# Kernel tuning notes

Measured on AMD Instinct MI355X. Metric: run time of the kernel, lower is better.

Reference implementation:

```python
import jax, jax.numpy as jnp
import numpy as np

N_GAUSS = 3200          # 20*20*8 voxel-center pseudo points
FEAT_DIM = 17
RENDER_H, RENDER_W = 48, 88
GT_H, GT_W = 192, 352
VOXEL_SIZE = 0.8
PC_MIN = np.array([-8.0, -8.0, -3.2], np.float32)
PC_MAX = np.array([8.0, 8.0, 3.2], np.float32)
NUSC_FREQ = np.array([1163161, 2309034, 188743, 2997643, 20317180, 852476, 243808,
                      2457947, 497017, 2731022, 7224789, 214411435, 5565043,
                      63191967, 76098082, 128860031, 141625221, 2307405309], np.float64)


def setup_inputs() -> dict:
    key = jax.random.key(0)
    k1, k2 = jax.random.split(key, 2)
    # pseudo voxel-center grid (get_presudo_xyz): cell centers on a 20x20x8 grid
    gx = (np.arange(20) + 0.5) * VOXEL_SIZE + PC_MIN[0]
    gy = (np.arange(20) + 0.5) * VOXEL_SIZE + PC_MIN[1]
    gz = (np.arange(8) + 0.5) * VOXEL_SIZE + PC_MIN[2]
    X, Y, Z = np.meshgrid(gx, gy, gz, indexing='ij')
    pc_xyz = np.stack([X, Y, Z], -1).reshape(-1, 3).astype(np.float32)
    # distCUDA2 on a regular grid: mean sq dist to 3 NNs == voxel_size^2
    scales = np.full((N_GAUSS, 3), np.log(VOXEL_SIZE), np.float32)  # log(sqrt(v^2))
    rots = np.zeros((N_GAUSS, 4), np.float32); rots[:, 0] = 1.0  # identity quats
    # two cameras looking at the grid (z_cam > 0 for all points)
    vm0 = np.array([[1, 0, 0, 0], [0, -1, 0, 0], [0, 0, -1, 20], [0, 0, 0, 1]], np.float32)
    vm1 = np.array([[0, 1, 0, 0], [0, 0, -1, 0], [-1, 0, 0, 20], [0, 0, 0, 1]], np.float32)
    viewmats = np.stack([vm0, vm1])
    intr = np.array([[100.0, 50.0, RENDER_W / 2.0, RENDER_H / 2.0]] * 2, np.float32)
    cw = (1.0 / np.log(NUSC_FREQ[:17] + 0.001)).astype(np.float32)
    return {
        'voxel_feats': jax.random.normal(k1, (1, N_GAUSS, FEAT_DIM), jnp.float32),
        'opacity': jax.random.uniform(k2, (1, N_GAUSS, 1), jnp.float32),
        'pc_xyz': jnp.asarray(pc_xyz),
        'scales': jnp.asarray(scales),
        'rots': jnp.asarray(rots),
        'viewmats': jnp.asarray(viewmats),
        'intrinsics': jnp.asarray(intr),
        'class_weights': jnp.asarray(cw),
        'gt_sem': jax.random.randint(jax.random.fold_in(key, 1), (2, GT_H, GT_W), 0, 17, jnp.int32),
        'sem_mask': jax.random.randint(jax.random.fold_in(key, 2), (2, GT_H, GT_W), 0, 2, jnp.int32),
    }


def quat_to_rot(q):
    q = q / jnp.linalg.norm(q, axis=-1, keepdims=True)
    w, x, y, z = q[:, 0], q[:, 1], q[:, 2], q[:, 3]
    return jnp.stack([
        jnp.stack([1 - 2 * (y * y + z * z), 2 * (x * y - w * z), 2 * (x * z + w * y)], -1),
        jnp.stack([2 * (x * y + w * z), 1 - 2 * (x * x + z * z), 2 * (y * z - w * x)], -1),
        jnp.stack([2 * (x * z - w * y), 2 * (y * z + w * x), 1 - 2 * (x * x + y * y)], -1),
    ], -2)  # [N,3,3]


def nearest_resize(img, H, W):
    hi, wi = img.shape
    ri = (jnp.arange(H) * hi) // H
    ci = (jnp.arange(W) * wi) // W
    return img[ri][:, ci]


def render_feature_map(feats, opac, xyz, scale, Rq, viewmat, intr):
    fx, fy, cx, cy = intr[0], intr[1], intr[2], intr[3]
    Rw, t = viewmat[:3, :3], viewmat[:3, 3]
    p = xyz @ Rw.T + t                      # [N,3] camera-frame
    z = p[:, 2]
    valid = z > 0.2
    zc = jnp.maximum(z, 0.2)
    u = fx * p[:, 0] / zc + cx
    v = fy * p[:, 1] / zc + cy
    # 3D covariance: Rq diag(s^2) Rq^T, then to camera frame
    cov3d = jnp.einsum('nij,nj,nkj->nik', Rq, scale * scale, Rq)
    cov_c = jnp.einsum('ij,njk,lk->nil', Rw, cov3d, Rw)
    # projection Jacobian (EWA splatting)
    zero = jnp.zeros_like(zc)
    J = jnp.stack([
        jnp.stack([fx / zc, zero, -fx * p[:, 0] / (zc * zc)], -1),
        jnp.stack([zero, fy / zc, -fy * p[:, 1] / (zc * zc)], -1),
    ], -2)                                  # [N,2,3]
    cov2 = jnp.einsum('nij,njk,nlk->nil', J, cov_c, J)
    a = cov2[:, 0, 0] + 0.3
    b = cov2[:, 0, 1]
    c = cov2[:, 1, 1] + 0.3
    det = jnp.maximum(a * c - b * b, 1e-8)
    A, B, C = c / det, -b / det, a / det    # conic
    px = jnp.arange(RENDER_W, dtype=jnp.float32)
    py = jnp.arange(RENDER_H, dtype=jnp.float32)
    dx = px[None, :] - u[:, None]           # [N,W]
    dy = py[None, :] - v[:, None]           # [N,H]
    power = (-0.5 * (A[:, None, None] * dx[:, None, :] ** 2
                     + C[:, None, None] * dy[:, :, None] ** 2)
             - B[:, None, None] * dx[:, None, :] * dy[:, :, None])  # [N,H,W]
    power = jnp.minimum(power, 0.0)
    alpha = jnp.clip(opac[:, None, None] * jnp.exp(power), 0.0, 0.99)
    alpha = alpha * valid[:, None, None].astype(alpha.dtype)
    order = jnp.argsort(z)                  # front-to-back depth sort
    alpha = alpha[order]
    feats_s = feats[order]
    T = jnp.cumprod(1.0 - alpha, axis=0)
    T_excl = jnp.concatenate([jnp.ones_like(T[:1]), T[:-1]], axis=0)
    w = alpha * T_excl                      # composite weights [N,H,W]
    return jnp.einsum('nhw,nc->hwc', w, feats_s)  # [H,W,17]


def masked_weighted_ce(logits, gt, mask, cw):
    logp = jax.nn.log_softmax(logits, -1)
    nll = -jnp.take_along_axis(logp, gt[:, None], axis=1)[:, 0]
    wi = cw[gt] * mask
    return jnp.sum(wi * nll) / jnp.maximum(jnp.sum(wi), 1e-8)


def reference(voxel_feats, opacity, pc_xyz, scales, rots, viewmats, intrinsics,
              class_weights, gt_sem, sem_mask):
    scale = jnp.exp(scales)
    Rq = quat_to_rot(rots)
    B = voxel_feats.shape[0]
    n_cam = viewmats.shape[0]
    loss_batch = 0.0
    for b in range(B):
        feats = voxel_feats[b].reshape(-1, FEAT_DIM)
        opac = opacity[b].reshape(-1)
        loss_cam = 0.0
        for c in range(n_cam):
            img = render_feature_map(feats, opac, pc_xyz, scale, Rq,
                                     viewmats[c], intrinsics[c])
            logits = img.reshape(-1, FEAT_DIM)
            gt = nearest_resize(gt_sem[c], RENDER_H, RENDER_W).reshape(-1)
            m = nearest_resize(sem_mask[c], RENDER_H, RENDER_W).reshape(-1).astype(jnp.float32)
            loss_cam = loss_cam + masked_weighted_ce(logits, gt, m, class_weights)
        loss_batch = loss_batch + loss_cam / n_cam
    return loss_batch / B  # gaussian_sem_weight = 1.0
```

## Files before the change

### kernel.cpp

```cpp
#include <hip/hip_runtime.h>

#define NG 3200
#define NF 17
#define NFP 18
#define RH 48
#define RW 88
#define NPIX (RH*RW)
#define GTH 192
#define GTW 352
#define NCAM 2
#define CHUNK 64
#define NCHUNK 50
#define GPC 5
#define NGROUP 10
#define NPL 9

typedef float v2f __attribute__((ext_vector_type(2)));
typedef _Float16 h2 __attribute__((ext_vector_type(2)));

#define Z_OFF    0
#define PU_OFF   (Z_OFF + NCAM*NG)
#define PS_OFF   (PU_OFF + NCAM*NG*6)
#define FS_OFF   (PS_OFF + NCAM*NG*6)
#define PT_OFF   (FS_OFF + NCAM*NG*NFP)
#define GP_OFF   (PT_OFF + NCAM*NCHUNK*NPL*NPIX)
#define ACC_OFF  (GP_OFF + NCAM*NGROUP*NPL*NPIX)

__global__ __launch_bounds__(256) void k_preproc(
    const float* __restrict__ opac, const float* __restrict__ xyz,
    const float* __restrict__ scales, const float* __restrict__ rots,
    const float* __restrict__ vm, const float* __restrict__ intr,
    float* __restrict__ ws)
{
  int idx = blockIdx.x*blockDim.x + threadIdx.x;
  if (idx < 4) ws[ACC_OFF + idx] = 0.0f;
  if (idx >= NCAM*NG) return;
  int cam = idx / NG, g = idx % NG;

  float qw=rots[g*4+0], qx=rots[g*4+1], qy=rots[g*4+2], qz=rots[g*4+3];
  float qn = rsqrtf(qw*qw+qx*qx+qy*qy+qz*qz);
  qw*=qn; qx*=qn; qy*=qn; qz*=qn;
  float R[3][3];
  R[0][0]=1.f-2.f*(qy*qy+qz*qz); R[0][1]=2.f*(qx*qy-qw*qz); R[0][2]=2.f*(qx*qz+qw*qy);
  R[1][0]=2.f*(qx*qy+qw*qz); R[1][1]=1.f-2.f*(qx*qx+qz*qz); R[1][2]=2.f*(qy*qz-qw*qx);
  R[2][0]=2.f*(qx*qz-qw*qy); R[2][1]=2.f*(qy*qz+qw*qx); R[2][2]=1.f-2.f*(qx*qx+qy*qy);

  float s2[3];
  #pragma unroll
  for (int k=0;k<3;k++){ float s=expf(scales[g*3+k]); s2[k]=s*s; }

  float M[3][3];
  #pragma unroll
  for(int i=0;i<3;i++)
    #pragma unroll
    for(int j=0;j<3;j++)
      M[i][j] = R[i][0]*s2[0]*R[j][0] + R[i][1]*s2[1]*R[j][1] + R[i][2]*s2[2]*R[j][2];

  const float* Vm = vm + cam*16;
  float Rw[3][3], t[3];
  #pragma unroll
  for(int i=0;i<3;i++){
    #pragma unroll
    for(int j=0;j<3;j++) Rw[i][j]=Vm[i*4+j];
    t[i]=Vm[i*4+3];
  }

  float T1[3][3];
  #pragma unroll
  for(int i=0;i<3;i++)
    #pragma unroll
    for(int j=0;j<3;j++)
      T1[i][j] = Rw[i][0]*M[0][j] + Rw[i][1]*M[1][j] + Rw[i][2]*M[2][j];
  float V[3][3];
  #pragma unroll
  for(int i=0;i<3;i++)
    #pragma unroll
    for(int j=0;j<3;j++)
      V[i][j] = T1[i][0]*Rw[j][0] + T1[i][1]*Rw[j][1] + T1[i][2]*Rw[j][2];

  float X=xyz[g*3+0], Y=xyz[g*3+1], Zp=xyz[g*3+2];
  float p0 = Rw[0][0]*X + Rw[0][1]*Y + Rw[0][2]*Zp + t[0];
  float p1 = Rw[1][0]*X + Rw[1][1]*Y + Rw[1][2]*Zp + t[1];
  float p2 = Rw[2][0]*X + Rw[2][1]*Y + Rw[2][2]*Zp + t[2];

  float z  = p2;
  float zc = fmaxf(z, 0.2f);
  float fx=intr[cam*4+0], fy=intr[cam*4+1], cx=intr[cam*4+2], cy=intr[cam*4+3];
  float u = fx*p0/zc + cx;
  float v = fy*p1/zc + cy;

  float j00 = fx/zc, j02 = -fx*p0/(zc*zc);
  float j11 = fy/zc, j12 = -fy*p1/(zc*zc);
  float c00 = j00*j00*V[0][0] + 2.f*j00*j02*V[0][2] + j02*j02*V[2][2];
  float c01 = j00*(V[0][1]*j11 + V[0][2]*j12) + j02*(V[2][1]*j11 + V[2][2]*j12);
  float c11 = j11*j11*V[1][1] + 2.f*j11*j12*V[1][2] + j12*j12*V[2][2];

  float a = c00 + 0.3f, b = c01, c = c11 + 0.3f;
  float det = fmaxf(a*c - b*b, 1e-8f);
  const float L2E = 1.4426950408889634f;
  float A2 = -0.5f*L2E * (c/det);
  float B2 = -L2E * (-b/det);
  float C2 = -0.5f*L2E * (a/det);
  float opv = (z > 0.2f) ? opac[g] : 0.0f;

  ws[Z_OFF + idx] = z;
  float* P = ws + PU_OFF + (size_t)idx*6;
  P[0]=u; P[1]=v; P[2]=A2; P[3]=B2; P[4]=C2; P[5]=opv;
}

__global__ __launch_bounds__(256) void k_sort(
    const float* __restrict__ feats, float* __restrict__ ws)
{
  __shared__ float zsh[NG];
  int cam = blockIdx.y;
  for (int i=threadIdx.x; i<NG; i+=256) zsh[i] = ws[Z_OFF + cam*NG + i];
  __syncthreads();

  int wave = threadIdx.x >> 6, lane = threadIdx.x & 63;
  int g = blockIdx.x*4 + wave;
  float zi = zsh[g];
  int rank = 0;
  #pragma unroll 5
  for (int k=0; k<NG/64; k++){
    int j = k*64 + lane;
    float zj = zsh[j];
    rank += ((zj < zi) || (zj == zi && j < g)) ? 1 : 0;
  }
  #pragma unroll
  for (int off=32; off>0; off>>=1) rank += __shfl_down(rank, off, 64);
  rank = __shfl(rank, 0, 64);

  const float* src = ws + PU_OFF + (size_t)(cam*NG+g)*6;
  if (lane < 6) (ws + PS_OFF + (size_t)(cam*NG+rank)*6)[lane] = src[lane];
  if (lane < NFP) (ws + FS_OFF + (size_t)(cam*NG+rank)*NFP)[lane] =
                     (lane < NF) ? feats[g*NF+lane] : 0.0f;
}

__global__ __launch_bounds__(192) void k_render(float* __restrict__ ws)
{
  __shared__ float sp[CHUNK*6];
  __shared__ v2f   sf2[CHUNK*(NFP/2)];
  int cam = blockIdx.z, chunk = blockIdx.y;
  int g0 = chunk*CHUNK;
  const float* psrc = ws + PS_OFF + (size_t)(cam*NG+g0)*6;
  for (int i=threadIdx.x; i<CHUNK*6; i+=192) sp[i]=psrc[i];
  const float* fsrc = ws + FS_OFF + (size_t)(cam*NG+g0)*NFP;
  float* sff = (float*)sf2;
  for (int i=threadIdx.x; i<CHUNK*NFP; i+=192) sff[i]=fsrc[i];
  __syncthreads();

  int pix = blockIdx.x*192 + threadIdx.x;
  float px = (float)(pix % RW), py = (float)(pix / RW);

  float T = 1.0f;
  v2f F2[9];
  #pragma unroll
  for(int k=0;k<9;k++) F2[k]=(v2f)(0.f);

  #pragma unroll 4
  for (int g=0; g<CHUNK; g++){
    const float* P = sp + g*6;
    float dx = px - P[0], dy = py - P[1];
    float m1 = P[2]*dx;
    float m2 = fmaf(P[3], dy, m1);
    float m3 = dx*m2;
    float power2 = fmaf(P[4]*dy, dy, m3);
    power2 = fminf(power2, 0.f);
    float alpha = fminf(P[5]*exp2f(power2), 0.99f);
    float w = alpha*T;
    T = fmaf(-alpha, T, T);
    v2f w2; w2.x = w; w2.y = w;
    const v2f* f2 = sf2 + g*(NFP/2);
    #pragma unroll
    for(int k=0;k<9;k++) F2[k] += w2*f2[k];
  }

  const float* Ff = (const float*)F2;
  h2* out = (h2*)(ws + PT_OFF) + (size_t)((cam*NCHUNK+chunk)*NPL)*NPIX + pix;
  #pragma unroll
  for(int k=0;k<8;k++){
    h2 v; v.x = (_Float16)Ff[2*k]; v.y = (_Float16)Ff[2*k+1];
    out[k*NPIX] = v;
  }
  { h2 v; v.x = (_Float16)Ff[16]; v.y = (_Float16)T; out[8*NPIX] = v; }
}

__global__ __launch_bounds__(192) void k_combine(float* __restrict__ ws)
{
  int cam = blockIdx.z, grp = blockIdx.y;
  int pix = blockIdx.x*192 + threadIdx.x;
  float F[NF];
  #pragma unroll
  for(int k=0;k<NF;k++) F[k]=0.f;
  float T = 1.f;
  for (int c=grp*GPC; c<grp*GPC+GPC; c++){
    const h2* base = (const h2*)(ws + PT_OFF) + (size_t)((cam*NCHUNK+c)*NPL)*NPIX + pix;
    h2 v[9];
    #pragma unroll
    for(int k=0;k<9;k++) v[k] = base[k*NPIX];
    #pragma unroll
    for(int k=0;k<8;k++){ F[2*k] += T*(float)v[k].x; F[2*k+1] += T*(float)v[k].y; }
    F[16] += T*(float)v[8].x;
    T *= (float)v[8].y;
  }
  h2* out = (h2*)(ws + GP_OFF) + (size_t)((cam*NGROUP+grp)*NPL)*NPIX + pix;
  #pragma unroll
  for(int k=0;k<8;k++){
    h2 v; v.x = (_Float16)F[2*k]; v.y = (_Float16)F[2*k+1];
    out[k*NPIX] = v;
  }
  { h2 v; v.x = (_Float16)F[16]; v.y = (_Float16)T; out[8*NPIX] = v; }
}

__global__ __launch_bounds__(192) void k_loss(
    const int* __restrict__ gt, const int* __restrict__ mask,
    const float* __restrict__ cw, float* __restrict__ ws)
{
  int cam = blockIdx.y;
  int pix = blockIdx.x*192 + threadIdx.x;
  float img[NF];
  #pragma unroll
  for(int k=0;k<NF;k++) img[k]=0.f;
  float Trun = 1.f;
  for (int c=0; c<NGROUP; c++){
    const h2* base = (const h2*)(ws + GP_OFF) + (size_t)((cam*NGROUP+c)*NPL)*NPIX + pix;
    h2 v[9];
    #pragma unroll
    for(int k=0;k<9;k++) v[k] = base[k*NPIX];
    #pragma unroll
    for(int k=0;k<8;k++){ img[2*k] += Trun*(float)v[k].x; img[2*k+1] += Trun*(float)v[k].y; }
    img[16] += Trun*(float)v[8].x;
    Trun *= (float)v[8].y;
  }
  int row = pix / RW, col = pix % RW;
  int gofs = cam*GTH*GTW + (row*4)*GTW + col*4;
  int gi = gt[gofs];
  float mi = (float)mask[gofs];
  float mx = img[0];
  #pragma unroll
  for(int k=1;k<NF;k++) mx = fmaxf(mx, img[k]);
  float s = 0.f;
  #pragma unroll
  for(int k=0;k<NF;k++) s += expf(img[k]-mx);
  float lse = mx + logf(s);
  float nll = lse - img[gi];
  float wi  = cw[gi]*mi;
  float num = wi*nll, den = wi;
  #pragma unroll
  for (int off=32; off>0; off>>=1){
    num += __shfl_down(num, off, 64);
    den += __shfl_down(den, off, 64);
  }
  if ((threadIdx.x & 63) == 0){
    atomicAdd(ws + ACC_OFF + cam*2 + 0, num);
    atomicAdd(ws + ACC_OFF + cam*2 + 1, den);
  }
}

__global__ void k_final(const float* __restrict__ ws, float* __restrict__ out)
{
  float l0 = ws[ACC_OFF+0]/fmaxf(ws[ACC_OFF+1], 1e-8f);
  float l1 = ws[ACC_OFF+2]/fmaxf(ws[ACC_OFF+3], 1e-8f);
  out[0] = 0.5f*(l0 + l1);
}

extern "C" void kernel_launch(void* const* d_in, const int* in_sizes, int n_in,
                              void* d_out, int out_size, void* d_ws, size_t ws_size,
                              hipStream_t stream) {
  const float* vf   = (const float*)d_in[0];
  const float* op   = (const float*)d_in[1];
  const float* xyz  = (const float*)d_in[2];
  const float* sc   = (const float*)d_in[3];
  const float* rt   = (const float*)d_in[4];
  const float* vm   = (const float*)d_in[5];
  const float* intr = (const float*)d_in[6];
  const float* cw   = (const float*)d_in[7];
  const int*   gt   = (const int*)d_in[8];
  const int*   mask = (const int*)d_in[9];
  float* ws  = (float*)d_ws;
  float* out = (float*)d_out;

  k_preproc<<<dim3((NCAM*NG+255)/256), 256, 0, stream>>>(op, xyz, sc, rt, vm, intr, ws);
  k_sort   <<<dim3(NG/4, NCAM), 256, 0, stream>>>(vf, ws);
  k_render <<<dim3(NPIX/192, NCHUNK, NCAM), 192, 0, stream>>>(ws);
  k_combine<<<dim3(NPIX/192, NGROUP, NCAM), 192, 0, stream>>>(ws);
  k_loss   <<<dim3(NPIX/192, NCAM), 192, 0, stream>>>(gt, mask, cw, ws);
  k_final  <<<1,1,0,stream>>>(ws, out);
}
```

Baseline: 130.5 us.

## Fuse combine, loss and final reduction into one kernel with last-block ticket

Merges the chunk-combine, loss and final kernels into a single kernel. Eight waves each composite five chunks, the partial results are merged in shared memory, and the final loss is written by the last block through an atomic ticket counter. Chunks grow from 64 to 80 Gaussians, giving 40 chunks instead of 50. This removes two launches and the fp16 round-trip of intermediate group partials, at the cost of a larger render per-chunk workload and a serial merge done by a single wave.

```diff
diff --git a/kernel.cpp b/kernel.cpp
--- a/kernel.cpp
+++ b/kernel.cpp
@@ -9,11 +9,11 @@
 #define GTH 192
 #define GTW 352
 #define NCAM 2
-#define CHUNK 64
-#define NCHUNK 50
-#define GPC 5
-#define NGROUP 10
+#define CHUNK 80
+#define NCHUNK 40
 #define NPL 9
+#define CPW 5
+#define NLOSSBLK (NPIX/64*NCAM)
 
 typedef float v2f __attribute__((ext_vector_type(2)));
 typedef _Float16 h2 __attribute__((ext_vector_type(2)));
@@ -23,8 +23,7 @@
 #define PS_OFF   (PU_OFF + NCAM*NG*6)
 #define FS_OFF   (PS_OFF + NCAM*NG*6)
 #define PT_OFF   (FS_OFF + NCAM*NG*NFP)
-#define GP_OFF   (PT_OFF + NCAM*NCHUNK*NPL*NPIX)
-#define ACC_OFF  (GP_OFF + NCAM*NGROUP*NPL*NPIX)
+#define ACC_OFF  (PT_OFF + NCAM*NCHUNK*NPL*NPIX)
 
 __global__ __launch_bounds__(256) void k_preproc(
     const float* __restrict__ opac, const float* __restrict__ xyz,
@@ -33,7 +32,7 @@
     float* __restrict__ ws)
 {
   int idx = blockIdx.x*blockDim.x + threadIdx.x;
-  if (idx < 4) ws[ACC_OFF + idx] = 0.0f;
+  if (idx < 8) ws[ACC_OFF + idx] = 0.0f;
   if (idx >= NCAM*NG) return;
   int cam = idx / NG, g = idx % NG;
 
@@ -185,15 +184,22 @@
   { h2 v; v.x = (_Float16)Ff[16]; v.y = (_Float16)T; out[8*NPIX] = v; }
 }
 
-__global__ __launch_bounds__(192) void k_combine(float* __restrict__ ws)
-{
-  int cam = blockIdx.z, grp = blockIdx.y;
-  int pix = blockIdx.x*192 + threadIdx.x;
+__global__ __launch_bounds__(512) void k_loss(
+    const int* __restrict__ gt, const int* __restrict__ mask,
+    const float* __restrict__ cw, float* __restrict__ ws, float* __restrict__ out)
+{
+  __shared__ float part[8*64*19];
+  int cam = blockIdx.y;
+  int wave = threadIdx.x >> 6, lane = threadIdx.x & 63;
+  int pix = blockIdx.x*64 + lane;
+
   float F[NF];
   #pragma unroll
   for(int k=0;k<NF;k++) F[k]=0.f;
   float T = 1.f;
-  for (int c=grp*GPC; c<grp*GPC+GPC; c++){
+  #pragma unroll
+  for (int i=0;i<CPW;i++){
+    int c = wave*CPW + i;
     const h2* base = (const h2*)(ws + PT_OFF) + (size_t)((cam*NCHUNK+c)*NPL)*NPIX + pix;
     h2 v[9];
     #pragma unroll
@@ -203,65 +209,58 @@
     F[16] += T*(float)v[8].x;
     T *= (float)v[8].y;
   }
-  h2* out = (h2*)(ws + GP_OFF) + (size_t)((cam*NGROUP+grp)*NPL)*NPIX + pix;
-  #pragma unroll
-  for(int k=0;k<8;k++){
-    h2 v; v.x = (_Float16)F[2*k]; v.y = (_Float16)F[2*k+1];
-    out[k*NPIX] = v;
-  }
-  { h2 v; v.x = (_Float16)F[16]; v.y = (_Float16)T; out[8*NPIX] = v; }
-}
-
-__global__ __launch_bounds__(192) void k_loss(
-    const int* __restrict__ gt, const int* __restrict__ mask,
-    const float* __restrict__ cw, float* __restrict__ ws)
-{
-  int cam = blockIdx.y;
-  int pix = blockIdx.x*192 + threadIdx.x;
-  float img[NF];
-  #pragma unroll
-  for(int k=0;k<NF;k++) img[k]=0.f;
-  float Trun = 1.f;
-  for (int c=0; c<NGROUP; c++){
-    const h2* base = (const h2*)(ws + GP_OFF) + (size_t)((cam*NGROUP+c)*NPL)*NPIX + pix;
-    h2 v[9];
-    #pragma unroll
-    for(int k=0;k<9;k++) v[k] = base[k*NPIX];
-    #pragma unroll
-    for(int k=0;k<8;k++){ img[2*k] += Trun*(float)v[k].x; img[2*k+1] += Trun*(float)v[k].y; }
-    img[16] += Trun*(float)v[8].x;
-    Trun *= (float)v[8].y;
-  }
-  int row = pix / RW, col = pix % RW;
-  int gofs = cam*GTH*GTW + (row*4)*GTW + col*4;
-  int gi = gt[gofs];
-  float mi = (float)mask[gofs];
-  float mx = img[0];
-  #pragma unroll
-  for(int k=1;k<NF;k++) mx = fmaxf(mx, img[k]);
-  float s = 0.f;
-  #pragma unroll
-  for(int k=0;k<NF;k++) s += expf(img[k]-mx);
-  float lse = mx + logf(s);
-  float nll = lse - img[gi];
-  float wi  = cw[gi]*mi;
-  float num = wi*nll, den = wi;
-  #pragma unroll
-  for (int off=32; off>0; off>>=1){
-    num += __shfl_down(num, off, 64);
-    den += __shfl_down(den, off, 64);
-  }
-  if ((threadIdx.x & 63) == 0){
-    atomicAdd(ws + ACC_OFF + cam*2 + 0, num);
-    atomicAdd(ws + ACC_OFF + cam*2 + 1, den);
-  }
-}
-
-__global__ void k_final(const float* __restrict__ ws, float* __restrict__ out)
-{
-  float l0 = ws[ACC_OFF+0]/fmaxf(ws[ACC_OFF+1], 1e-8f);
-  float l1 = ws[ACC_OFF+2]/fmaxf(ws[ACC_OFF+3], 1e-8f);
-  out[0] = 0.5f*(l0 + l1);
+  float* p = part + (wave*64 + lane)*19;
+  #pragma unroll
+  for(int k=0;k<NF;k++) p[k]=F[k];
+  p[17]=T;
+  __syncthreads();
+
+  if (wave == 0){
+    float img[NF];
+    #pragma unroll
+    for(int k=0;k<NF;k++) img[k]=0.f;
+    float Trun = 1.f;
+    for (int w=0; w<8; w++){
+      const float* b = part + (w*64 + lane)*19;
+      #pragma unroll
+      for(int k=0;k<NF;k++) img[k] += Trun*b[k];
+      Trun *= b[17];
+    }
+    int row = pix / RW, col = pix % RW;
+    int gofs = cam*GTH*GTW + (row*4)*GTW + col*4;
+    int gi = gt[gofs];
+    float mi = (float)mask[gofs];
+    float mx = img[0];
+    #pragma unroll
+    for(int k=1;k<NF;k++) mx = fmaxf(mx, img[k]);
+    float s = 0.f;
+    #pragma unroll
+    for(int k=0;k<NF;k++) s += expf(img[k]-mx);
+    float lse = mx + logf(s);
+    float nll = lse - img[gi];
+    float wi  = cw[gi]*mi;
+    float num = wi*nll, den = wi;
+    #pragma unroll
+    for (int off=32; off>0; off>>=1){
+      num += __shfl_down(num, off, 64);
+      den += __shfl_down(den, off, 64);
+    }
+    if (lane == 0){
+      atomicAdd(ws + ACC_OFF + cam*2 + 0, num);
+      atomicAdd(ws + ACC_OFF + cam*2 + 1, den);
+      __threadfence();
+      int ticket = (int)atomicAdd(ws + ACC_OFF + 4, 1.0f);
+      if (ticket == NLOSSBLK-1){
+        float n0 = atomicAdd(ws + ACC_OFF + 0, 0.f);
+        float d0 = atomicAdd(ws + ACC_OFF + 1, 0.f);
+        float n1 = atomicAdd(ws + ACC_OFF + 2, 0.f);
+        float d1 = atomicAdd(ws + ACC_OFF + 3, 0.f);
+        float l0 = n0/fmaxf(d0, 1e-8f);
+        float l1 = n1/fmaxf(d1, 1e-8f);
+        out[0] = 0.5f*(l0 + l1);
+      }
+    }
+  }
 }
 
 extern "C" void kernel_launch(void* const* d_in, const int* in_sizes, int n_in,
@@ -283,7 +282,5 @@
   k_preproc<<<dim3((NCAM*NG+255)/256), 256, 0, stream>>>(op, xyz, sc, rt, vm, intr, ws);
   k_sort   <<<dim3(NG/4, NCAM), 256, 0, stream>>>(vf, ws);
   k_render <<<dim3(NPIX/192, NCHUNK, NCAM), 192, 0, stream>>>(ws);
-  k_combine<<<dim3(NPIX/192, NGROUP, NCAM), 192, 0, stream>>>(ws);
-  k_loss   <<<dim3(NPIX/192, NCAM), 192, 0, stream>>>(gt, mask, cw, ws);
-  k_final  <<<1,1,0,stream>>>(ws, out);
-}
+  k_loss   <<<dim3(NPIX/64, NCAM), 512, 0, stream>>>(gt, mask, cw, ws, out);
+}
```

Measured after the change: 125.9 us. 3.5% less time.
